# Performance work log

Measured on AMD Instinct MI355X. Metric: run time of the kernel, lower is better.

## Reference

```python
import jax, jax.numpy as jnp
from jax import lax
import numpy as np

V, D, H, K = 50000, 300, 256, 37  # vocab, emb dim, lstm hidden, num_tags
B, T = 64, 256


def setup_inputs() -> dict:
    key = jax.random.key(0)
    ks = jax.random.split(key, 24)
    lengths = jax.random.randint(ks[0], (B,), T // 2, T + 1)
    valid = jnp.arange(T)[None, :] < lengths[:, None]
    text = jnp.where(valid, jax.random.randint(ks[1], (B, T), 1, V), 0)
    sbj = jax.random.randint(ks[2], (B, T), 0, K)

    def p(k, shape, s=0.05):
        return jax.random.normal(k, shape, jnp.float32) * s

    return {
        "text": text, "sbj": sbj,
        "emb": p(ks[3], (V, D), 0.1),
        # layer 0 (input D=300), forward + backward directions, torch gate order i,f,g,o
        "Wih0f": p(ks[4], (4 * H, D)), "Whh0f": p(ks[5], (4 * H, H)), "b0f": jnp.zeros((4 * H,), jnp.float32),
        "Wih0b": p(ks[6], (4 * H, D)), "Whh0b": p(ks[7], (4 * H, H)), "b0b": jnp.zeros((4 * H,), jnp.float32),
        # layer 1 (input 2H=512)
        "Wih1f": p(ks[8], (4 * H, 2 * H)), "Whh1f": p(ks[9], (4 * H, H)), "b1f": jnp.zeros((4 * H,), jnp.float32),
        "Wih1b": p(ks[10], (4 * H, 2 * H)), "Whh1b": p(ks[11], (4 * H, H)), "b1b": jnp.zeros((4 * H,), jnp.float32),
        "W_sbj": p(ks[12], (K, 2 * H)), "b_sbj": jnp.zeros((K,), jnp.float32),
        # CRF params (torchcrf init: uniform(-0.1, 0.1))
        "start_t": p(ks[13], (K,), 0.1), "end_t": p(ks[14], (K,), 0.1), "trans": p(ks[15], (K, K), 0.1),
    }


def _lstm(x, Wih, Whh, b, reverse):
    # x: [T, B, Din] time-major; returns hidden states [T, B, H]
    Bn, Hn = x.shape[1], Whh.shape[1]

    def step(carry, xt):
        h, c = carry
        z = xt @ Wih.T + h @ Whh.T + b
        i, f, g, o = jnp.split(z, 4, axis=-1)
        c = jax.nn.sigmoid(f) * c + jax.nn.sigmoid(i) * jnp.tanh(g)
        h = jax.nn.sigmoid(o) * jnp.tanh(c)
        return (h, c), h

    init = (jnp.zeros((Bn, Hn), x.dtype), jnp.zeros((Bn, Hn), x.dtype))
    return lax.scan(step, init, x, reverse=reverse)[1]


def reference(text, sbj, emb, Wih0f, Whh0f, b0f, Wih0b, Whh0b, b0b,
              Wih1f, Whh1f, b1f, Wih1b, Whh1b, b1b,
              W_sbj, b_sbj, start_t, end_t, trans):
    mask = (text != 0)                      # [B, T]
    x = jnp.transpose(emb[text], (1, 0, 2))  # [T, B, D]
    h0 = jnp.concatenate([_lstm(x, Wih0f, Whh0f, b0f, False),
                          _lstm(x, Wih0b, Whh0b, b0b, True)], axis=-1)   # [T, B, 2H]
    h1 = jnp.concatenate([_lstm(h0, Wih1f, Whh1f, b1f, False),
                          _lstm(h0, Wih1b, Whh1b, b1b, True)], axis=-1)  # [T, B, 2H]
    em = h1 @ W_sbj.T + b_sbj               # emissions [T, B, K]

    tags = sbj.T                            # [T, B]
    m = mask.T                              # [T, B]
    mf = m.astype(em.dtype)

    # --- numerator: score of the gold path ---
    em_sel = jnp.take_along_axis(em, tags[:, :, None], axis=2)[..., 0]  # [T, B]
    tr_sel = trans[tags[:-1], tags[1:]]                                  # [T-1, B]
    seq_ends = m.sum(0) - 1
    last_tags = tags[seq_ends, jnp.arange(tags.shape[1])]
    num = (start_t[tags[0]] + em_sel[0]
           + jnp.sum((em_sel[1:] + tr_sel) * mf[1:], axis=0)
           + end_t[last_tags])              # [B]

    # --- log partition: forward algorithm (logsumexp DP over K tags) ---
    def step(score, inp):
        em_t, m_t = inp
        nxt = jax.scipy.special.logsumexp(
            score[:, :, None] + trans[None, :, :] + em_t[:, None, :], axis=1)
        return jnp.where(m_t[:, None], nxt, score), None

    score0 = start_t[None, :] + em[0]       # [B, K]
    score = lax.scan(step, score0, (em[1:], m[1:]))[0]
    logZ = jax.scipy.special.logsumexp(score + end_t[None, :], axis=-1)  # [B]

    llh = num - logZ
    return -(llh.sum() / mf.sum())          # -1 * token_mean log-likelihood
```

## Files before the change

kernel.cpp:

```cpp
#include <hip/hip_runtime.h>
#include <math.h>

#define TT 256
#define BB 64
#define DD 300
#define KP0 320
#define HH 256
#define KK 37
#define FH 1024
#define MTOT (TT*BB)

typedef __attribute__((ext_vector_type(8))) short short8;
typedef __attribute__((ext_vector_type(4))) float f32x4;

__device__ __forceinline__ float bf2f(unsigned short u) {
    union { float f; unsigned int i; } v; v.i = ((unsigned int)u) << 16; return v.f;
}
__device__ __forceinline__ unsigned short f2bf(float f) {
    union { float f; unsigned int i; } v; v.f = f;
    unsigned int i = v.i;
    unsigned int r = (i + 0x7FFFu + ((i >> 16) & 1u)) >> 16;
    return (unsigned short)r;
}
__device__ __forceinline__ float sigm(float x)   { return 1.0f / (1.0f + __expf(-x)); }
__device__ __forceinline__ float tanh_f(float x) { return 2.0f / (1.0f + __expf(-2.0f * x)) - 1.0f; }

__device__ __forceinline__ int sb0(int w) { return (w << 24) >> 24; }
__device__ __forceinline__ int sb1(int w) { return (w << 16) >> 24; }
__device__ __forceinline__ int sb2(int w) { return (w <<  8) >> 24; }
__device__ __forceinline__ int sb3(int w) { return  w        >> 24; }

#if defined(__has_builtin)
#if __has_builtin(__builtin_amdgcn_sdot4)
#define HAVE_SDOT4 1
#endif
#endif

__device__ __forceinline__ int dot4i8(int a, int b, int c) {
#ifdef HAVE_SDOT4
    return __builtin_amdgcn_sdot4(a, b, c, false);
#else
    return c + sb0(a) * sb0(b) + sb1(a) * sb1(b) + sb2(a) * sb2(b) + sb3(a) * sb3(b);
#endif
}

__device__ __forceinline__ void lstm_dot(int hw, int4 wv, int& a0, int& a1, int& a2, int& a3) {
    a0 = dot4i8(hw, wv.x, a0);
    a1 = dot4i8(hw, wv.y, a1);
    a2 = dot4i8(hw, wv.z, a2);
    a3 = dot4i8(hw, wv.w, a3);
}

__device__ __forceinline__ int perm_col(int nn) { return ((nn & 255) << 2) | (nn >> 8); }

__global__ __launch_bounds__(64) void conv_scale(
    const float* __restrict__ w0f, const float* __restrict__ w0b,
    const float* __restrict__ w1f, const float* __restrict__ w1b,
    float* __restrict__ S)
{
    const int m = blockIdx.x >> 10;
    const int r = blockIdx.x & 1023;
    const float* W = m == 0 ? w0f : m == 1 ? w0b : m == 2 ? w1f : w1b;
    const int t = threadIdx.x;
    float mx = 0.f;
    for (int k = t; k < HH; k += 64) mx = fmaxf(mx, fabsf(W[r * HH + k]));
    #pragma unroll
    for (int s = 32; s > 0; s >>= 1) mx = fmaxf(mx, __shfl_down(mx, s, 64));
    if (t == 0) {
        const int g = r >> 8, u = r & 255;
        S[m * 1024 + u * 4 + g] = fmaxf(mx, 1e-20f) / 127.0f;
    }
}

__global__ __launch_bounds__(256) void conv_wq(
    const float* __restrict__ w0f, const float* __restrict__ w0b,
    const float* __restrict__ w1f, const float* __restrict__ w1b,
    const float* __restrict__ S, unsigned int* __restrict__ WQ)
{
    const int idx = blockIdx.x * 256 + threadIdx.x;
    const int m = idx >> 16;
    const int r = idx & 65535;
    const float* W = m == 0 ? w0f : m == 1 ? w0b : m == 2 ? w1f : w1b;
    const int g  = r & 3;
    const int u  = (r >> 2) & 255;
    const int j  = (r >> 10) & 15;
    const int kq = r >> 14;
    const int k0 = kq * 64 + j * 4;
    const float s = S[m * 1024 + u * 4 + g];
    const float4 wv = *(const float4*)(W + (g * HH + u) * HH + k0);
    int q0 = (int)rintf(wv.x / s), q1 = (int)rintf(wv.y / s);
    int q2 = (int)rintf(wv.z / s), q3 = (int)rintf(wv.w / s);
    q0 = max(-127, min(127, q0)); q1 = max(-127, min(127, q1));
    q2 = max(-127, min(127, q2)); q3 = max(-127, min(127, q3));
    WQ[idx] = (unsigned int)(q0 & 0xff) | ((unsigned int)(q1 & 0xff) << 8) |
              ((unsigned int)(q2 & 0xff) << 16) | ((unsigned int)(q3 & 0xff) << 24);
}

__global__ __launch_bounds__(256) void conv_wsbj(
    const float* __restrict__ Wsbj, float* __restrict__ WT)
{
    const int idx = blockIdx.x * 256 + threadIdx.x;
    if (idx >= 512 * KK) return;
    const int c = idx / KK, k = idx - c * KK;
    WT[idx] = Wsbj[k * 512 + c];
}

__global__ __launch_bounds__(320) void conv_gather(
    const int* __restrict__ text, const float* __restrict__ emb,
    unsigned short* __restrict__ Abf)
{
    const int r = blockIdx.x;
    const int k = threadIdx.x;
    const int t = r >> 6, b = r & 63;
    const int idx = text[b * TT + t];
    Abf[r * KP0 + k] = (k < DD) ? f2bf(emb[(size_t)idx * DD + k]) : (unsigned short)0;
}

__global__ __launch_bounds__(256) void conv_w(
    const float* __restrict__ src, unsigned short* __restrict__ dst,
    int kin, int kout, int total)
{
    const int idx = blockIdx.x * 256 + threadIdx.x;
    if (idx >= total) return;
    const int rr = idx / kout, k = idx - rr * kout;
    dst[idx] = (k < kin) ? f2bf(src[rr * kin + k]) : (unsigned short)0;
}

__global__ __launch_bounds__(256) void gemm_mfma(
    const unsigned short* __restrict__ A,
    const unsigned short* __restrict__ W,
    const float* __restrict__ bias,
    unsigned short* __restrict__ out,
    int lda)
{
    const int bm = blockIdx.x * 128;
    const int bn = blockIdx.y * 128;
    const int tid = threadIdx.x;
    const int lane = tid & 63;
    const int wave = tid >> 6;
    const int wm = (wave & 1) * 64;
    const int wn = (wave >> 1) * 64;

    __shared__ __align__(16) unsigned short As[128 * 32];
    __shared__ __align__(16) unsigned short Bs[128 * 32];

    f32x4 acc[4][4] = {};

    const int srow = tid >> 2;
    const int sk = (tid & 3) * 8;

    const unsigned short* ga0 = A + (size_t)(bm + srow) * lda + sk;
    const unsigned short* ga1 = A + (size_t)(bm + srow + 64) * lda + sk;
    const unsigned short* gb0 = W + (size_t)(bn + srow) * lda + sk;
    const unsigned short* gb1 = W + (size_t)(bn + srow + 64) * lda + sk;

    unsigned short* lA0 = As + wave * 512;
    unsigned short* lA1 = As + 2048 + wave * 512;
    unsigned short* lB0 = Bs + wave * 512;
    unsigned short* lB1 = Bs + 2048 + wave * 512;

    const int kiters = lda >> 5;
    for (int kb = 0; kb < kiters; kb++) {
        const int k0 = kb * 32;
        __builtin_amdgcn_global_load_lds(
            (const __attribute__((address_space(1))) unsigned int*)(ga0 + k0),
            (__attribute__((address_space(3))) unsigned int*)lA0, 16, 0, 0);
        __builtin_amdgcn_global_load_lds(
            (const __attribute__((address_space(1))) unsigned int*)(ga1 + k0),
            (__attribute__((address_space(3))) unsigned int*)lA1, 16, 0, 0);
        __builtin_amdgcn_global_load_lds(
            (const __attribute__((address_space(1))) unsigned int*)(gb0 + k0),
            (__attribute__((address_space(3))) unsigned int*)lB0, 16, 0, 0);
        __builtin_amdgcn_global_load_lds(
            (const __attribute__((address_space(1))) unsigned int*)(gb1 + k0),
            (__attribute__((address_space(3))) unsigned int*)lB1, 16, 0, 0);
        __syncthreads();

        short8 af[4], bfr[4];
        #pragma unroll
        for (int i = 0; i < 4; i++) {
            af[i]  = *(const short8*)&As[(wm + i * 16 + (lane & 15)) * 32 + (lane >> 4) * 8];
            bfr[i] = *(const short8*)&Bs[(wn + i * 16 + (lane & 15)) * 32 + (lane >> 4) * 8];
        }
        #pragma unroll
        for (int i = 0; i < 4; i++)
            #pragma unroll
            for (int j = 0; j < 4; j++)
                acc[i][j] = __builtin_amdgcn_mfma_f32_16x16x32_bf16(af[i], bfr[j], acc[i][j], 0, 0, 0);
        __syncthreads();
    }

    const int cn = lane & 15;
    const int cr = (lane >> 4) * 4;
    #pragma unroll
    for (int j = 0; j < 4; j++) {
        const int n = bn + wn + j * 16 + cn;
        const float bv = bias[n];
        const int pc = perm_col(n);
        #pragma unroll
        for (int i = 0; i < 4; i++) {
            #pragma unroll
            for (int r = 0; r < 4; r++) {
                const int m = bm + wm + i * 16 + cr + r;
                out[(size_t)m * FH + pc] = f2bf(acc[i][j][r] + bv);
            }
        }
    }
}

__global__ __launch_bounds__(1024, 4) void lstm_kernel(
    const unsigned short* __restrict__ zin_f, const unsigned short* __restrict__ zin_b,
    const int* __restrict__ WQf, const int* __restrict__ WQb,
    const float* __restrict__ Sf, const float* __restrict__ Sb,
    unsigned short* __restrict__ h_out)
{
    const int dir = blockIdx.y;
    const unsigned short* zin = dir ? zin_b : zin_f;
    const int*   WQ = dir ? WQb : WQf;
    const float* S  = dir ? Sb  : Sf;
    const int off = dir ? HH : 0;

    const int b = blockIdx.x;
    const int tid = threadIdx.x;
    const int u  = tid & 255;
    const int kq = tid >> 8;

    __shared__ __align__(16) unsigned char hq8[2][HH];
    __shared__ int4 red[3][HH];

    const int4* wp = (const int4*)WQ + kq * 16 * 256 + u;
    const int4 w0  = wp[ 0 * 256], w1  = wp[ 1 * 256], w2  = wp[ 2 * 256], w3  = wp[ 3 * 256];
    const int4 w4  = wp[ 4 * 256], w5  = wp[ 5 * 256], w6  = wp[ 6 * 256], w7  = wp[ 7 * 256];
    const int4 w8  = wp[ 8 * 256], w9  = wp[ 9 * 256], w10 = wp[10 * 256], w11 = wp[11 * 256];
    const int4 w12 = wp[12 * 256], w13 = wp[13 * 256], w14 = wp[14 * 256], w15 = wp[15 * 256];

    float4 sc = make_float4(0.f, 0.f, 0.f, 0.f);
    if (kq == 0) {
        sc = *(const float4*)(S + 4 * u);
        const float inv127 = 1.0f / 127.0f;
        sc.x *= inv127; sc.y *= inv127; sc.z *= inv127; sc.w *= inv127;
    }
    float c = 0.0f;
    int cur = 0;
    if (tid < 128) ((unsigned int*)hq8)[tid] = 0u;
    __syncthreads();

    for (int ts = 0; ts < TT; ts++) {
        const int tt = dir ? (TT - 1 - ts) : ts;
        const int row = tt * BB + b;

        ushort4 zv = make_ushort4(0, 0, 0, 0);
        if (kq == 0) zv = *(const ushort4*)(zin + row * FH + 4 * u);

        const int4* hv = (const int4*)&hq8[cur][kq * 64];
        const int4 hA = hv[0], hB = hv[1], hC = hv[2], hD = hv[3];

        int a0 = 0, a1 = 0, a2 = 0, a3 = 0;
        lstm_dot(hA.x, w0,  a0, a1, a2, a3);
        lstm_dot(hA.y, w1,  a0, a1, a2, a3);
        lstm_dot(hA.z, w2,  a0, a1, a2, a3);
        lstm_dot(hA.w, w3,  a0, a1, a2, a3);
        lstm_dot(hB.x, w4,  a0, a1, a2, a3);
        lstm_dot(hB.y, w5,  a0, a1, a2, a3);
        lstm_dot(hB.z, w6,  a0, a1, a2, a3);
        lstm_dot(hB.w, w7,  a0, a1, a2, a3);
        lstm_dot(hC.x, w8,  a0, a1, a2, a3);
        lstm_dot(hC.y, w9,  a0, a1, a2, a3);
        lstm_dot(hC.z, w10, a0, a1, a2, a3);
        lstm_dot(hC.w, w11, a0, a1, a2, a3);
        lstm_dot(hD.x, w12, a0, a1, a2, a3);
        lstm_dot(hD.y, w13, a0, a1, a2, a3);
        lstm_dot(hD.z, w14, a0, a1, a2, a3);
        lstm_dot(hD.w, w15, a0, a1, a2, a3);

        if (kq) red[kq - 1][u] = make_int4(a0, a1, a2, a3);
        __syncthreads();

        if (kq == 0) {
            const int4 r0 = red[0][u], r1 = red[1][u], r2 = red[2][u];
            const int A0 = a0 + r0.x + r1.x + r2.x;
            const int A1 = a1 + r0.y + r1.y + r2.y;
            const int A2 = a2 + r0.z + r1.z + r2.z;
            const int A3 = a3 + r0.w + r1.w + r2.w;
            const float zi  = (float)A0 * sc.x + bf2f(zv.x);
            const float zf_ = (float)A1 * sc.y + bf2f(zv.y);
            const float zg  = (float)A2 * sc.z + bf2f(zv.z);
            const float zo  = (float)A3 * sc.w + bf2f(zv.w);
            const float cc = sigm(zf_) * c + sigm(zi) * tanh_f(zg);
            c = cc;
            const float hh = sigm(zo) * tanh_f(cc);
            hq8[cur ^ 1][u] = (unsigned char)((int)rintf(hh * 127.0f));
            h_out[row * (2 * HH) + off + u] = f2bf(hh);
        }
        __syncthreads();
        cur ^= 1;
    }
}

__global__ __launch_bounds__(256) void em_kernel(
    const unsigned short* __restrict__ h1, const float* __restrict__ WsbjT,
    const float* __restrict__ bsbj, float* __restrict__ em)
{
    const int o = blockIdx.x * 256 + threadIdx.x;
    if (o >= MTOT * KK) return;
    const int r = o / KK, k = o - r * KK;
    const unsigned short* hr = h1 + r * 512;
    float s = bsbj[k];
    #pragma unroll 4
    for (int cidx = 0; cidx < 512; cidx++) {
        s += bf2f(hr[cidx]) * WsbjT[cidx * KK + k];
    }
    em[o] = s;
}

__global__ __launch_bounds__(64) void crf_kernel(
    const int* __restrict__ text, const int* __restrict__ sbj,
    const float* __restrict__ em,
    const float* __restrict__ start_t, const float* __restrict__ end_t,
    const float* __restrict__ trans, float* __restrict__ accum)
{
    const int b = blockIdx.x;
    const int tid = threadIdx.x;
    __shared__ float tr[KK * KK];
    __shared__ float sc[2][KK];
    for (int x = tid; x < KK * KK; x += 64) tr[x] = trans[x];

    int cnt = 0;
    for (int t = tid; t < TT; t += 64) cnt += (text[b * TT + t] != 0) ? 1 : 0;
    #pragma unroll
    for (int s = 32; s > 0; s >>= 1) cnt += __shfl_down(cnt, s, 64);
    const int len = __shfl(cnt, 0, 64);

    __syncthreads();

    float part = 0.f;
    for (int t = tid; t < TT; t += 64) {
        if (t >= 1 && t < len) {
            const int tg = sbj[b * TT + t];
            const int tp = sbj[b * TT + t - 1];
            part += em[(t * BB + b) * KK + tg] + tr[tp * KK + tg];
        }
    }
    #pragma unroll
    for (int s = 32; s > 0; s >>= 1) part += __shfl_down(part, s, 64);

    if (tid < KK) sc[0][tid] = start_t[tid] + em[b * KK + tid];
    __syncthreads();
    int cur = 0;
    for (int t = 1; t < len; t++) {
        float nv = 0.f;
        if (tid < KK) {
            float mx = -1e30f;
            for (int k1 = 0; k1 < KK; k1++)
                mx = fmaxf(mx, sc[cur][k1] + tr[k1 * KK + tid]);
            float s = 0.f;
            for (int k1 = 0; k1 < KK; k1++)
                s += __expf(sc[cur][k1] + tr[k1 * KK + tid] - mx);
            nv = mx + __logf(s) + em[(t * BB + b) * KK + tid];
        }
        if (tid < KK) sc[cur ^ 1][tid] = nv;
        __syncthreads();
        cur ^= 1;
    }

    if (tid == 0) {
        const int tg0 = sbj[b * TT];
        const int tgl = sbj[b * TT + len - 1];
        const float num = start_t[tg0] + em[b * KK + tg0] + part + end_t[tgl];
        float mx = -1e30f;
        for (int k = 0; k < KK; k++) mx = fmaxf(mx, sc[cur][k] + end_t[k]);
        float s = 0.f;
        for (int k = 0; k < KK; k++) s += __expf(sc[cur][k] + end_t[k] - mx);
        const float logZ = mx + __logf(s);
        atomicAdd(&accum[0], num - logZ);
        atomicAdd(&accum[1], (float)len);
    }
}

__global__ void init_kernel(float* __restrict__ accum) {
    if (threadIdx.x < 2) accum[threadIdx.x] = 0.0f;
}
__global__ void final_kernel(const float* __restrict__ accum, float* __restrict__ out) {
    out[0] = -(accum[0] / accum[1]);
}

extern "C" void kernel_launch(void* const* d_in, const int* in_sizes, int n_in,
                              void* d_out, int out_size, void* d_ws, size_t ws_size,
                              hipStream_t stream)
{
    (void)in_sizes; (void)n_in; (void)out_size; (void)ws_size;
    const int*   text  = (const int*)d_in[0];
    const int*   sbj   = (const int*)d_in[1];
    const float* emb   = (const float*)d_in[2];
    const float* Wih0f = (const float*)d_in[3];
    const float* Whh0f = (const float*)d_in[4];
    const float* b0f   = (const float*)d_in[5];
    const float* Wih0b = (const float*)d_in[6];
    const float* Whh0b = (const float*)d_in[7];
    const float* b0b   = (const float*)d_in[8];
    const float* Wih1f = (const float*)d_in[9];
    const float* Whh1f = (const float*)d_in[10];
    const float* b1f   = (const float*)d_in[11];
    const float* Wih1b = (const float*)d_in[12];
    const float* Whh1b = (const float*)d_in[13];
    const float* b1b   = (const float*)d_in[14];
    const float* Wsbj  = (const float*)d_in[15];
    const float* bsbj  = (const float*)d_in[16];
    const float* start_t = (const float*)d_in[17];
    const float* end_t   = (const float*)d_in[18];
    const float* trans   = (const float*)d_in[19];

    char* ws = (char*)d_ws;
    unsigned short* zf   = (unsigned short*)(ws + 0);
    unsigned short* zb   = (unsigned short*)(ws + 33554432);
    unsigned short* h0   = (unsigned short*)(ws + 67108864);
    unsigned short* h1   = (unsigned short*)(ws + 83886080);
    unsigned short* Wb0f = (unsigned short*)(ws + 67108864);
    unsigned short* Wb0b = (unsigned short*)(ws + 67764224);
    unsigned short* Abf  = (unsigned short*)(ws + 83886080);
    unsigned short* Wb1f = (unsigned short*)(ws + 94371840);
    unsigned short* Wb1b = (unsigned short*)(ws + 95420416);
    unsigned int*   WQ   = (unsigned int*)(ws + 100663296);
    float*          Sq   = (float*)(ws + 101711872);
    float*        WsbjT  = (float*)(ws + 102760448);
    float*          acc  = (float*)(ws + 102836224);
    float*           em  = (float*)(ws + 0);
    float* out = (float*)d_out;

    const int* WQ0f = (const int*)(WQ + 0 * 65536);
    const int* WQ0b = (const int*)(WQ + 1 * 65536);
    const int* WQ1f = (const int*)(WQ + 2 * 65536);
    const int* WQ1b = (const int*)(WQ + 3 * 65536);
    const float* S0f = Sq + 0 * 1024;
    const float* S0b = Sq + 1 * 1024;
    const float* S1f = Sq + 2 * 1024;
    const float* S1b = Sq + 3 * 1024;

    init_kernel<<<1, 64, 0, stream>>>(acc);
    conv_scale<<<dim3(4096), 64, 0, stream>>>(Whh0f, Whh0b, Whh1f, Whh1b, Sq);
    conv_wq<<<dim3(1024), 256, 0, stream>>>(Whh0f, Whh0b, Whh1f, Whh1b, Sq, WQ);
    conv_wsbj<<<dim3(74), 256, 0, stream>>>(Wsbj, WsbjT);
    conv_gather<<<dim3(MTOT), 320, 0, stream>>>(text, emb, Abf);
    conv_w<<<dim3(1280), 256, 0, stream>>>(Wih0f, Wb0f, DD, KP0, 1024 * KP0);
    conv_w<<<dim3(1280), 256, 0, stream>>>(Wih0b, Wb0b, DD, KP0, 1024 * KP0);
    conv_w<<<dim3(2048), 256, 0, stream>>>(Wih1f, Wb1f, 512, 512, 1024 * 512);
    conv_w<<<dim3(2048), 256, 0, stream>>>(Wih1b, Wb1b, 512, 512, 1024 * 512);

    gemm_mfma<<<dim3(128, 8), 256, 0, stream>>>(Abf, Wb0f, b0f, zf, KP0);
    gemm_mfma<<<dim3(128, 8), 256, 0, stream>>>(Abf, Wb0b, b0b, zb, KP0);
    lstm_kernel<<<dim3(BB, 2), 1024, 0, stream>>>(zf, zb, WQ0f, WQ0b, S0f, S0b, h0);
    gemm_mfma<<<dim3(128, 8), 256, 0, stream>>>(h0, Wb1f, b1f, zf, 512);
    gemm_mfma<<<dim3(128, 8), 256, 0, stream>>>(h0, Wb1b, b1b, zb, 512);
    lstm_kernel<<<dim3(BB, 2), 1024, 0, stream>>>(zf, zb, WQ1f, WQ1b, S1f, S1b, h1);

    em_kernel<<<(MTOT * KK + 255) / 256, 256, 0, stream>>>(h1, WsbjT, bsbj, em);
    crf_kernel<<<BB, 64, 0, stream>>>(text, sbj, em, start_t, end_t, trans, acc);
    final_kernel<<<1, 1, 0, stream>>>(acc, out);
}
```

Before: 1.153 ms.

## Hold full recurrent weights per thread in LSTM and use MFMA for emissions

The LSTM kernel drops from 1024 to 256 threads per block. Each thread now keeps all 64 int4 packed int8 weight words in registers, so the cross-thread reduction through shared memory and one barrier per step go away. The next step's input gate preactivations are prefetched while the current step computes. Separately, the scalar emission projection is replaced by a bf16 MFMA GEMM with padded transposed weights. The risks are heavy register pressure (256 VGPRs for weights) that may cause spills, and a serial dot length per thread four times longer than before.

```diff
diff --git a/kernel.cpp b/kernel.cpp
--- a/kernel.cpp
+++ b/kernel.cpp
@@ -96,13 +96,13 @@
               ((unsigned int)(q2 & 0xff) << 16) | ((unsigned int)(q3 & 0xff) << 24);
 }
 
-__global__ __launch_bounds__(256) void conv_wsbj(
-    const float* __restrict__ Wsbj, float* __restrict__ WT)
+__global__ __launch_bounds__(256) void conv_wsbj_bf(
+    const float* __restrict__ Wsbj, unsigned short* __restrict__ WB)
 {
     const int idx = blockIdx.x * 256 + threadIdx.x;
-    if (idx >= 512 * KK) return;
-    const int c = idx / KK, k = idx - c * KK;
-    WT[idx] = Wsbj[k * 512 + c];
+    if (idx >= 64 * 512) return;
+    const int r = idx >> 9, cidx = idx & 511;
+    WB[idx] = (r < KK) ? f2bf(Wsbj[r * 512 + cidx]) : (unsigned short)0;
 }
 
 __global__ __launch_bounds__(320) void conv_gather(
@@ -208,7 +208,83 @@
     }
 }
 
-__global__ __launch_bounds__(1024, 4) void lstm_kernel(
+__global__ __launch_bounds__(256) void gemm_em(
+    const unsigned short* __restrict__ A,
+    const unsigned short* __restrict__ W,
+    const float* __restrict__ bias,
+    float* __restrict__ em)
+{
+    const int bm = blockIdx.x * 128;
+    const int tid = threadIdx.x;
+    const int lane = tid & 63;
+    const int wave = tid >> 6;
+    const int wm = (wave & 1) * 64;
+    const int wn = (wave >> 1) * 32;
+
+    __shared__ __align__(16) unsigned short As[128 * 32];
+    __shared__ __align__(16) unsigned short Bs[64 * 32];
+
+    f32x4 acc[4][2] = {};
+
+    const int srow = tid >> 2;
+    const int sk = (tid & 3) * 8;
+
+    const unsigned short* ga0 = A + (size_t)(bm + srow) * 512 + sk;
+    const unsigned short* ga1 = A + (size_t)(bm + srow + 64) * 512 + sk;
+    const unsigned short* gb  = W + (size_t)srow * 512 + sk;
+
+    unsigned short* lA0 = As + wave * 512;
+    unsigned short* lA1 = As + 2048 + wave * 512;
+    unsigned short* lB  = Bs + wave * 512;
+
+    for (int kb = 0; kb < 16; kb++) {
+        const int k0 = kb * 32;
+        __builtin_amdgcn_global_load_lds(
+            (const __attribute__((address_space(1))) unsigned int*)(ga0 + k0),
+            (__attribute__((address_space(3))) unsigned int*)lA0, 16, 0, 0);
+        __builtin_amdgcn_global_load_lds(
+            (const __attribute__((address_space(1))) unsigned int*)(ga1 + k0),
+            (__attribute__((address_space(3))) unsigned int*)lA1, 16, 0, 0);
+        __builtin_amdgcn_global_load_lds(
+            (const __attribute__((address_space(1))) unsigned int*)(gb + k0),
+            (__attribute__((address_space(3))) unsigned int*)lB, 16, 0, 0);
+        __syncthreads();
+
+        short8 af[4], bfr[2];
+        #pragma unroll
+        for (int i = 0; i < 4; i++)
+            af[i]  = *(const short8*)&As[(wm + i * 16 + (lane & 15)) * 32 + (lane >> 4) * 8];
+        #pragma unroll
+        for (int j = 0; j < 2; j++)
+            bfr[j] = *(const short8*)&Bs[(wn + j * 16 + (lane & 15)) * 32 + (lane >> 4) * 8];
+        #pragma unroll
+        for (int i = 0; i < 4; i++)
+            #pragma unroll
+            for (int j = 0; j < 2; j++)
+                acc[i][j] = __builtin_amdgcn_mfma_f32_16x16x32_bf16(af[i], bfr[j], acc[i][j], 0, 0, 0);
+        __syncthreads();
+    }
+
+    const int cn = lane & 15;
+    const int cr = (lane >> 4) * 4;
+    #pragma unroll
+    for (int j = 0; j < 2; j++) {
+        const int n = wn + j * 16 + cn;
+        if (n < KK) {
+            const float bv = bias[n];
+            #pragma unroll
+            for (int i = 0; i < 4; i++) {
+                #pragma unroll
+                for (int r = 0; r < 4; r++) {
+                    const int m = bm + wm + i * 16 + cr + r;
+                    em[(size_t)m * KK + n] = acc[i][j][r] + bv;
+                }
+            }
+        }
+    }
+}
+
+__global__ __launch_bounds__(256, 1) void lstm_kernel(
     const unsigned short* __restrict__ zin_f, const unsigned short* __restrict__ zin_b,
     const int* __restrict__ WQf, const int* __restrict__ WQb,
     const float* __restrict__ Sf, const float* __restrict__ Sb,
@@ -221,96 +297,61 @@
     const int off = dir ? HH : 0;
 
     const int b = blockIdx.x;
-    const int tid = threadIdx.x;
-    const int u  = tid & 255;
-    const int kq = tid >> 8;
+    const int u = threadIdx.x;
 
     __shared__ __align__(16) unsigned char hq8[2][HH];
-    __shared__ int4 red[3][HH];
-
-    const int4* wp = (const int4*)WQ + kq * 16 * 256 + u;
-    const int4 w0  = wp[ 0 * 256], w1  = wp[ 1 * 256], w2  = wp[ 2 * 256], w3  = wp[ 3 * 256];
-    const int4 w4  = wp[ 4 * 256], w5  = wp[ 5 * 256], w6  = wp[ 6 * 256], w7  = wp[ 7 * 256];
-    const int4 w8  = wp[ 8 * 256], w9  = wp[ 9 * 256], w10 = wp[10 * 256], w11 = wp[11 * 256];
-    const int4 w12 = wp[12 * 256], w13 = wp[13 * 256], w14 = wp[14 * 256], w15 = wp[15 * 256];
-
-    float4 sc = make_float4(0.f, 0.f, 0.f, 0.f);
-    if (kq == 0) {
-        sc = *(const float4*)(S + 4 * u);
+
+    int4 w[64];
+    #pragma unroll
+    for (int j = 0; j < 64; j++) w[j] = ((const int4*)WQ)[j * 256 + u];
+
+    float4 sc = *(const float4*)(S + 4 * u);
+    {
         const float inv127 = 1.0f / 127.0f;
         sc.x *= inv127; sc.y *= inv127; sc.z *= inv127; sc.w *= inv127;
     }
     float c = 0.0f;
     int cur = 0;
-    if (tid < 128) ((unsigned int*)hq8)[tid] = 0u;
+    if (u < 128) ((unsigned int*)hq8)[u] = 0u;
     __syncthreads();
 
+    ushort4 zv;
+    {
+        const int tt0 = dir ? (TT - 1) : 0;
+        zv = *(const ushort4*)(zin + (tt0 * BB + b) * FH + 4 * u);
+    }
+
     for (int ts = 0; ts < TT; ts++) {
+        const int ts_n = (ts + 1 < TT) ? (ts + 1) : ts;
+        const int tt_n = dir ? (TT - 1 - ts_n) : ts_n;
+        const ushort4 zv_n = *(const ushort4*)(zin + (tt_n * BB + b) * FH + 4 * u);
+
+        const int4* hv = (const int4*)&hq8[cur][0];
+        int a0 = 0, a1 = 0, a2 = 0, a3 = 0;
+        #pragma unroll
+        for (int jq = 0; jq < 16; jq++) {
+            const int4 hw = hv[jq];
+            lstm_dot(hw.x, w[4 * jq + 0], a0, a1, a2, a3);
+            lstm_dot(hw.y, w[4 * jq + 1], a0, a1, a2, a3);
+            lstm_dot(hw.z, w[4 * jq + 2], a0, a1, a2, a3);
+            lstm_dot(hw.w, w[4 * jq + 3], a0, a1, a2, a3);
+        }
+
         const int tt = dir ? (TT - 1 - ts) : ts;
         const int row = tt * BB + b;
-
-        ushort4 zv = make_ushort4(0, 0, 0, 0);
-        if (kq == 0) zv = *(const ushort4*)(zin + row * FH + 4 * u);
-
-        const int4* hv = (const int4*)&hq8[cur][kq * 64];
-        const int4 hA = hv[0], hB = hv[1], hC = hv[2], hD = hv[3];
-
-        int a0 = 0, a1 = 0, a2 = 0, a3 = 0;
-        lstm_dot(hA.x, w0,  a0, a1, a2, a3);
-        lstm_dot(hA.y, w1,  a0, a1, a2, a3);
-        lstm_dot(hA.z, w2,  a0, a1, a2, a3);
-        lstm_dot(hA.w, w3,  a0, a1, a2, a3);
-        lstm_dot(hB.x, w4,  a0, a1, a2, a3);
-        lstm_dot(hB.y, w5,  a0, a1, a2, a3);
-        lstm_dot(hB.z, w6,  a0, a1, a2, a3);
-        lstm_dot(hB.w, w7,  a0, a1, a2, a3);
-        lstm_dot(hC.x, w8,  a0, a1, a2, a3);
-        lstm_dot(hC.y, w9,  a0, a1, a2, a3);
-        lstm_dot(hC.z, w10, a0, a1, a2, a3);
-        lstm_dot(hC.w, w11, a0, a1, a2, a3);
-        lstm_dot(hD.x, w12, a0, a1, a2, a3);
-        lstm_dot(hD.y, w13, a0, a1, a2, a3);
-        lstm_dot(hD.z, w14, a0, a1, a2, a3);
-        lstm_dot(hD.w, w15, a0, a1, a2, a3);
-
-        if (kq) red[kq - 1][u] = make_int4(a0, a1, a2, a3);
-        __syncthreads();
-
-        if (kq == 0) {
-            const int4 r0 = red[0][u], r1 = red[1][u], r2 = red[2][u];
-            const int A0 = a0 + r0.x + r1.x + r2.x;
-            const int A1 = a1 + r0.y + r1.y + r2.y;
-            const int A2 = a2 + r0.z + r1.z + r2.z;
-            const int A3 = a3 + r0.w + r1.w + r2.w;
-            const float zi  = (float)A0 * sc.x + bf2f(zv.x);
-            const float zf_ = (float)A1 * sc.y + bf2f(zv.y);
-            const float zg  = (float)A2 * sc.z + bf2f(zv.z);
-            const float zo  = (float)A3 * sc.w + bf2f(zv.w);
-            const float cc = sigm(zf_) * c + sigm(zi) * tanh_f(zg);
-            c = cc;
-            const float hh = sigm(zo) * tanh_f(cc);
-            hq8[cur ^ 1][u] = (unsigned char)((int)rintf(hh * 127.0f));
-            h_out[row * (2 * HH) + off + u] = f2bf(hh);
-        }
+        const float zi  = (float)a0 * sc.x + bf2f(zv.x);
+        const float zf_ = (float)a1 * sc.y + bf2f(zv.y);
+        const float zg  = (float)a2 * sc.z + bf2f(zv.z);
+        const float zo  = (float)a3 * sc.w + bf2f(zv.w);
+        const float cc = sigm(zf_) * c + sigm(zi) * tanh_f(zg);
+        c = cc;
+        const float hh = sigm(zo) * tanh_f(cc);
+        hq8[cur ^ 1][u] = (unsigned char)((int)rintf(hh * 127.0f));
+        h_out[row * (2 * HH) + off + u] = f2bf(hh);
         __syncthreads();
         cur ^= 1;
-    }
-}
-
-__global__ __launch_bounds__(256) void em_kernel(
-    const unsigned short* __restrict__ h1, const float* __restrict__ WsbjT,
-    const float* __restrict__ bsbj, float* __restrict__ em)
-{
-    const int o = blockIdx.x * 256 + threadIdx.x;
-    if (o >= MTOT * KK) return;
-    const int r = o / KK, k = o - r * KK;
-    const unsigned short* hr = h1 + r * 512;
-    float s = bsbj[k];
-    #pragma unroll 4
-    for (int cidx = 0; cidx < 512; cidx++) {
-        s += bf2f(hr[cidx]) * WsbjT[cidx * KK + k];
-    }
-    em[o] = s;
+        zv = zv_n;
+    }
 }
 
 __global__ __launch_bounds__(64) void crf_kernel(
@@ -422,7 +463,7 @@
     unsigned short* Wb1b = (unsigned short*)(ws + 95420416);
     unsigned int*   WQ   = (unsigned int*)(ws + 100663296);
     float*          Sq   = (float*)(ws + 101711872);
-    float*        WsbjT  = (float*)(ws + 102760448);
+    unsigned short* WsbjB = (unsigned short*)(ws + 102760448);
     float*          acc  = (float*)(ws + 102836224);
     float*           em  = (float*)(ws + 0);
     float* out = (float*)d_out;
@@ -439,7 +480,7 @@
     init_kernel<<<1, 64, 0, stream>>>(acc);
     conv_scale<<<dim3(4096), 64, 0, stream>>>(Whh0f, Whh0b, Whh1f, Whh1b, Sq);
     conv_wq<<<dim3(1024), 256, 0, stream>>>(Whh0f, Whh0b, Whh1f, Whh1b, Sq, WQ);
-    conv_wsbj<<<dim3(74), 256, 0, stream>>>(Wsbj, WsbjT);
+    conv_wsbj_bf<<<dim3(128), 256, 0, stream>>>(Wsbj, WsbjB);
     conv_gather<<<dim3(MTOT), 320, 0, stream>>>(text, emb, Abf);
     conv_w<<<dim3(1280), 256, 0, stream>>>(Wih0f, Wb0f, DD, KP0, 1024 * KP0);
     conv_w<<<dim3(1280), 256, 0, stream>>>(Wih0b, Wb0b, DD, KP0, 1024 * KP0);
@@ -448,12 +489,13 @@
 
     gemm_mfma<<<dim3(128, 8), 256, 0, stream>>>(Abf, Wb0f, b0f, zf, KP0);
     gemm_mfma<<<dim3(128, 8), 256, 0, stream>>>(Abf, Wb0b, b0b, zb, KP0);
-    lstm_kernel<<<dim3(BB, 2), 1024, 0, stream>>>(zf, zb, WQ0f, WQ0b, S0f, S0b, h0);
+    lstm_kernel<<<dim3(BB, 2), 256, 0, stream>>>(zf, zb, WQ0f, WQ0b, S0f, S0b, h0);
     gemm_mfma<<<dim3(128, 8), 256, 0, stream>>>(h0, Wb1f, b1f, zf, 512);
     gemm_mfma<<<dim3(128, 8), 256, 0, stream>>>(h0, Wb1b, b1b, zb, 512);
-    lstm_kernel<<<dim3(BB, 2), 1024, 0, stream>>>(zf, zb, WQ1f, WQ1b, S1f, S1b, h1);
-
-    em_kernel<<<(MTOT * KK + 255) / 256, 256, 0, stream>>>(h1, WsbjT, bsbj, em);
+    lstm_kernel<<<dim3(BB, 2), 256, 0, stream>>>(zf, zb, WQ1f, WQ1b, S1f, S1b, h1);
+
+    em_gemm_launch:
+    gemm_em<<<dim3(128), 256, 0, stream>>>(h1, WsbjB, bsbj, em);
     crf_kernel<<<BB, 64, 0, stream>>>(text, sbj, em, start_t, end_t, trans, acc);
     final_kernel<<<1, 1, 0, stream>>>(acc, out);
 }
```

Result: slower. 1.365 ms (+18.3%).
